# Performance work log

Hardware: AMD Instinct MI355X
Metric: run time of the kernel (lower is better)

Reference implementation:

```python
import jax, jax.numpy as jnp
import numpy as np

BLOCK_SIZE = 128  # init_kwargs block_size


def setup_inputs() -> dict:
    key = jax.random.key(0)
    kq, kk, kv = jax.random.split(key, 3)
    shape = (8, 16, 4096, 128)  # [B, H, L, D]
    q = jax.random.normal(kq, shape, dtype=jnp.float32)
    k = jax.random.normal(kk, shape, dtype=jnp.float32)
    v = jax.random.normal(kv, shape, dtype=jnp.float32)
    return {"q": q, "k": k, "v": v}


def reference(q, k, v):
    # Block-diagonal local attention. The torch code builds a dense [L,L]
    # score matrix filled with -10000 off the block diagonal; exp(-10000)
    # underflows to exactly 0 in fp32 after max-subtraction, so the dense
    # softmax is mathematically identical to per-block softmax. We honor
    # the block sparsity and never materialize the L x L matrix.
    w = BLOCK_SIZE
    B, H, L, D = q.shape
    nb = L // w
    qb = q.reshape(B, H, nb, w, D)
    kb = k.reshape(B, H, nb, w, D)
    vb = v.reshape(B, H, nb, w, D)
    # NOTE: original applies NO 1/sqrt(D) scaling.
    score = jnp.einsum('bhnwd,bhnud->bhnwu', qb, kb)   # [B,H,nb,w,w]
    probs = jax.nn.softmax(score, axis=-1)
    out = jnp.einsum('bhnwu,bhnud->bhnwd', probs, vb)
    return out.reshape(B, H, L, D)
```

## Files before the change

kernel.cpp:

```cpp
#include <hip/hip_runtime.h>

typedef _Float16 half8  __attribute__((ext_vector_type(8)));
typedef _Float16 half4v __attribute__((ext_vector_type(4)));
typedef float    f32x4  __attribute__((ext_vector_type(4)));

__device__ __forceinline__ int swz(int row) {
    return ((row ^ (row >> 3)) & 15) << 4;
}

__global__ __launch_bounds__(512, 8) void battn_kernel(
    const float* __restrict__ Q, const float* __restrict__ K,
    const float* __restrict__ V, float* __restrict__ O)
{
    __shared__ __align__(16) char smem[32768];
    const int tid  = threadIdx.x;
    const int lane = tid & 63;
    const int w    = tid >> 6;
    const int la   = lane & 15;
    const int u    = lane >> 4;
    const size_t base = (size_t)blockIdx.x * (128 * 128);

    const float* Qb = Q + base;
    const float* Kb = K + base;
    const float* Vb = V + base;
    float*       Ob = O + base;

    float4 kreg[8];
#pragma unroll
    for (int it = 0; it < 8; ++it)
        kreg[it] = *(const float4*)(Kb + it * 2048 + tid * 4);

    half8 qfrag[4];
    {
        const float* qrow = Qb + (w * 16 + la) * 128;
#pragma unroll
        for (int kk = 0; kk < 4; ++kk) {
            const float4 a = *(const float4*)(qrow + kk * 32 + u * 8);
            const float4 b = *(const float4*)(qrow + kk * 32 + u * 8 + 4);
            qfrag[kk][0] = (_Float16)a.x; qfrag[kk][1] = (_Float16)a.y;
            qfrag[kk][2] = (_Float16)a.z; qfrag[kk][3] = (_Float16)a.w;
            qfrag[kk][4] = (_Float16)b.x; qfrag[kk][5] = (_Float16)b.y;
            qfrag[kk][6] = (_Float16)b.z; qfrag[kk][7] = (_Float16)b.w;
        }
    }
#pragma unroll
    for (int it = 0; it < 8; ++it) {
        const int idx = it * 2048 + tid * 4;
        const int row = idx >> 7;
        const int col = idx & 127;
        half4v h;
        h[0] = (_Float16)kreg[it].x; h[1] = (_Float16)kreg[it].y;
        h[2] = (_Float16)kreg[it].z; h[3] = (_Float16)kreg[it].w;
        int byte = row * 256 + col * 2;
        byte ^= swz(row);
        *(half4v*)(smem + byte) = h;
    }
    __syncthreads();

    f32x4 acc[8];
#pragma unroll
    for (int t = 0; t < 8; ++t) acc[t] = (f32x4){0.f, 0.f, 0.f, 0.f};
#pragma unroll
    for (int t = 0; t < 8; ++t) {
#pragma unroll
        for (int kk = 0; kk < 4; ++kk) {
            const int row = t * 16 + la;
            int byte = row * 256 + kk * 64 + u * 16;
            byte ^= swz(row);
            const half8 kf = *(const half8*)(smem + byte);
            acc[t] = __builtin_amdgcn_mfma_f32_16x16x32_f16(qfrag[kk], kf, acc[t], 0, 0, 0);
        }
    }

    float inv[4];
#pragma unroll
    for (int r = 0; r < 4; ++r) {
        float m = acc[0][r];
#pragma unroll
        for (int t = 1; t < 8; ++t) m = fmaxf(m, acc[t][r]);
        m = fmaxf(m, __shfl_xor(m, 1));
        m = fmaxf(m, __shfl_xor(m, 2));
        m = fmaxf(m, __shfl_xor(m, 4));
        m = fmaxf(m, __shfl_xor(m, 8));
        float s = 0.f;
#pragma unroll
        for (int t = 0; t < 8; ++t) {
            const float e = __expf(acc[t][r] - m);
            acc[t][r] = e;
            s += e;
        }
        s += __shfl_xor(s, 1);
        s += __shfl_xor(s, 2);
        s += __shfl_xor(s, 4);
        s += __shfl_xor(s, 8);
        inv[r] = 1.0f / s;
    }

    __syncthreads();

#pragma unroll
    for (int t = 0; t < 8; ++t) {
#pragma unroll
        for (int r = 0; r < 4; ++r) {
            const int q   = w * 16 + u * 4 + r;
            const int col = t * 16 + la;
            int byte = q * 256 + col * 2;
            byte ^= swz(q & 15);
            *(_Float16*)(smem + byte) = (_Float16)(acc[t][r] * inv[r]);
        }
    }

    float vld[32];
#pragma unroll
    for (int kk = 0; kk < 4; ++kk)
#pragma unroll
        for (int i = 0; i < 8; ++i)
            vld[kk * 8 + i] = Vb[(kk * 32 + u * 8 + i) * 128 + w * 16 + la];

    __syncthreads();

    half8 vfrag[4];
#pragma unroll
    for (int kk = 0; kk < 4; ++kk)
#pragma unroll
        for (int i = 0; i < 8; ++i)
            vfrag[kk][i] = (_Float16)vld[kk * 8 + i];

#pragma unroll
    for (int qt = 0; qt < 8; ++qt) {
        half8 pb[4];
#pragma unroll
        for (int kk = 0; kk < 4; ++kk) {
            int byte = (qt * 16 + la) * 256 + kk * 64 + u * 16;
            byte ^= swz(la);
            pb[kk] = *(const half8*)(smem + byte);
        }
        f32x4 oa = (f32x4){0.f, 0.f, 0.f, 0.f};
#pragma unroll
        for (int kk = 0; kk < 4; ++kk)
            oa = __builtin_amdgcn_mfma_f32_16x16x32_f16(vfrag[kk], pb[kk], oa, 0, 0, 0);
        *(float4*)(Ob + (qt * 16 + la) * 128 + w * 16 + u * 4) =
            make_float4(oa[0], oa[1], oa[2], oa[3]);
    }
}

extern "C" void kernel_launch(void* const* d_in, const int* in_sizes, int n_in,
                              void* d_out, int out_size, void* d_ws, size_t ws_size,
                              hipStream_t stream) {
    const float* q = (const float*)d_in[0];
    const float* k = (const float*)d_in[1];
    const float* v = (const float*)d_in[2];
    float* o = (float*)d_out;
    const int nblocks = in_sizes[0] / (128 * 128);
    battn_kernel<<<dim3(nblocks), dim3(512), 0, stream>>>(q, k, v, o);
}
```

Baseline: 211.7 us.

## Load K directly to LDS in fp32 via global_load_lds and issue V loads early

K is now copied from global memory straight into LDS as fp32 with global_load_lds, using a swizzled source address, instead of staging through registers and converting to fp16 before the LDS write. The conversion to fp16 moves into the QK^T fragment read. V loads are issued earlier with inline asm, before the probability write to LDS, and awaited with an explicit vmcnt wait so their latency overlaps the softmax store. LDS doubles to 64KB and launch bounds drop to 4 blocks, which lowers occupancy and doubles LDS read traffic for K.

```diff
diff --git a/kernel.cpp b/kernel.cpp
--- a/kernel.cpp
+++ b/kernel.cpp
@@ -1,18 +1,17 @@
 #include <hip/hip_runtime.h>
 
 typedef _Float16 half8  __attribute__((ext_vector_type(8)));
-typedef _Float16 half4v __attribute__((ext_vector_type(4)));
 typedef float    f32x4  __attribute__((ext_vector_type(4)));
 
-__device__ __forceinline__ int swz(int row) {
+__device__ __forceinline__ int swzp(int row) {
     return ((row ^ (row >> 3)) & 15) << 4;
 }
 
-__global__ __launch_bounds__(512, 8) void battn_kernel(
+__global__ __launch_bounds__(512, 4) void battn_kernel(
     const float* __restrict__ Q, const float* __restrict__ K,
     const float* __restrict__ V, float* __restrict__ O)
 {
-    __shared__ __align__(16) char smem[32768];
+    __shared__ __align__(16) char smem[65536];
     const int tid  = threadIdx.x;
     const int lane = tid & 63;
     const int w    = tid >> 6;
@@ -25,36 +24,39 @@
     const float* Vb = V + base;
     float*       Ob = O + base;
 
-    float4 kreg[8];
-#pragma unroll
-    for (int it = 0; it < 8; ++it)
-        kreg[it] = *(const float4*)(Kb + it * 2048 + tid * 4);
-
-    half8 qfrag[4];
+    float4 qld[8];
     {
         const float* qrow = Qb + (w * 16 + la) * 128;
 #pragma unroll
         for (int kk = 0; kk < 4; ++kk) {
-            const float4 a = *(const float4*)(qrow + kk * 32 + u * 8);
-            const float4 b = *(const float4*)(qrow + kk * 32 + u * 8 + 4);
-            qfrag[kk][0] = (_Float16)a.x; qfrag[kk][1] = (_Float16)a.y;
-            qfrag[kk][2] = (_Float16)a.z; qfrag[kk][3] = (_Float16)a.w;
-            qfrag[kk][4] = (_Float16)b.x; qfrag[kk][5] = (_Float16)b.y;
-            qfrag[kk][6] = (_Float16)b.z; qfrag[kk][7] = (_Float16)b.w;
+            qld[2 * kk]     = *(const float4*)(qrow + kk * 32 + u * 8);
+            qld[2 * kk + 1] = *(const float4*)(qrow + kk * 32 + u * 8 + 4);
         }
     }
+
 #pragma unroll
     for (int it = 0; it < 8; ++it) {
-        const int idx = it * 2048 + tid * 4;
-        const int row = idx >> 7;
-        const int col = idx & 127;
-        half4v h;
-        h[0] = (_Float16)kreg[it].x; h[1] = (_Float16)kreg[it].y;
-        h[2] = (_Float16)kreg[it].z; h[3] = (_Float16)kreg[it].w;
-        int byte = row * 256 + col * 2;
-        byte ^= swz(row);
-        *(half4v*)(smem + byte) = h;
+        const int dst  = (w * 8 + it) * 1024 + lane * 16;
+        const int row  = dst >> 9;
+        const int x    = dst & 511;
+        const int srcf = row * 128 + ((x ^ ((row & 31) << 4)) >> 2);
+        __builtin_amdgcn_global_load_lds(
+            (const __attribute__((address_space(1))) void*)(Kb + srcf),
+            (__attribute__((address_space(3))) void*)(smem + (w * 8 + it) * 1024),
+            16, 0, 0);
     }
+
+    half8 qfrag[4];
+#pragma unroll
+    for (int kk = 0; kk < 4; ++kk) {
+        const float4 a = qld[2 * kk];
+        const float4 b = qld[2 * kk + 1];
+        qfrag[kk][0] = (_Float16)a.x; qfrag[kk][1] = (_Float16)a.y;
+        qfrag[kk][2] = (_Float16)a.z; qfrag[kk][3] = (_Float16)a.w;
+        qfrag[kk][4] = (_Float16)b.x; qfrag[kk][5] = (_Float16)b.y;
+        qfrag[kk][6] = (_Float16)b.z; qfrag[kk][7] = (_Float16)b.w;
+    }
+
     __syncthreads();
 
     f32x4 acc[8];
@@ -62,12 +64,19 @@
     for (int t = 0; t < 8; ++t) acc[t] = (f32x4){0.f, 0.f, 0.f, 0.f};
 #pragma unroll
     for (int t = 0; t < 8; ++t) {
+        const int row   = t * 16 + la;
+        const int rbase = row * 512;
+        const int sw    = (row & 31) << 4;
 #pragma unroll
         for (int kk = 0; kk < 4; ++kk) {
-            const int row = t * 16 + la;
-            int byte = row * 256 + kk * 64 + u * 16;
-            byte ^= swz(row);
-            const half8 kf = *(const half8*)(smem + byte);
+            const int c0 = kk * 128 + u * 32;
+            const float4 a = *(const float4*)(smem + rbase + (c0 ^ sw));
+            const float4 b = *(const float4*)(smem + rbase + ((c0 + 16) ^ sw));
+            half8 kf;
+            kf[0] = (_Float16)a.x; kf[1] = (_Float16)a.y;
+            kf[2] = (_Float16)a.z; kf[3] = (_Float16)a.w;
+            kf[4] = (_Float16)b.x; kf[5] = (_Float16)b.y;
+            kf[6] = (_Float16)b.z; kf[7] = (_Float16)b.w;
             acc[t] = __builtin_amdgcn_mfma_f32_16x16x32_f16(qfrag[kk], kf, acc[t], 0, 0, 0);
         }
     }
@@ -98,6 +107,19 @@
 
     __syncthreads();
 
+    float vld[32];
+    {
+        const float* vbase = Vb + w * 16 + la;
+#pragma unroll
+        for (int kk = 0; kk < 4; ++kk)
+#pragma unroll
+            for (int i = 0; i < 8; ++i) {
+                const float* p = vbase + (kk * 32 + u * 8 + i) * 128;
+                asm volatile("global_load_dword %0, %1, off"
+                             : "=v"(vld[kk * 8 + i]) : "v"(p));
+            }
+    }
+
 #pragma unroll
     for (int t = 0; t < 8; ++t) {
 #pragma unroll
@@ -105,19 +127,14 @@
             const int q   = w * 16 + u * 4 + r;
             const int col = t * 16 + la;
             int byte = q * 256 + col * 2;
-            byte ^= swz(q & 15);
+            byte ^= swzp(q & 15);
             *(_Float16*)(smem + byte) = (_Float16)(acc[t][r] * inv[r]);
         }
     }
+    __syncthreads();
 
-    float vld[32];
-#pragma unroll
-    for (int kk = 0; kk < 4; ++kk)
-#pragma unroll
-        for (int i = 0; i < 8; ++i)
-            vld[kk * 8 + i] = Vb[(kk * 32 + u * 8 + i) * 128 + w * 16 + la];
-
-    __syncthreads();
+    asm volatile("s_waitcnt vmcnt(0)" ::: "memory");
+    __builtin_amdgcn_sched_barrier(0);
 
     half8 vfrag[4];
 #pragma unroll
@@ -132,7 +149,7 @@
 #pragma unroll
         for (int kk = 0; kk < 4; ++kk) {
             int byte = (qt * 16 + la) * 256 + kk * 64 + u * 16;
-            byte ^= swz(la);
+            byte ^= swzp(la);
             pb[kk] = *(const half8*)(smem + byte);
         }
         f32x4 oa = (f32x4){0.f, 0.f, 0.f, 0.f};
```

Result: slower. 217.3 us (+2.6%).
